# Optimization experiments

Hardware: AMD Instinct MI355X
Metric: run time of the kernel (lower is better)

The kernel has to match this reference:

```python
import jax, jax.numpy as jnp
import numpy as np

B, T, C, E = 16, 392, 512, 512
E8 = E // 8          # dim_project output
K = T // 2           # top_k / number of sampled positions
RECEPTIVE_FIELD = 2.0


def setup_inputs() -> dict:
    key = jax.random.key(0)
    ks = jax.random.split(key, 6)
    s = 0.03  # trunc_normal std used by the module init
    return {
        "x_in": jax.random.normal(ks[0], (B, T, C), jnp.float32),
        "W_dim": jax.random.normal(ks[1], (E8, E), jnp.float32) * s,
        "b_dim": jnp.zeros((E8,), jnp.float32),
        "W_time": jax.random.normal(ks[2], (T, T * T), jnp.float32) * s,
        "b_time": jnp.zeros((T,), jnp.float32),
        "W_offa": jax.random.normal(ks[3], (K, T), jnp.float32) * s,
        "W_offd": jax.random.normal(ks[4], (K, T), jnp.float32) * s,
    }


def _grid_sample_1d(x, idx_norm):
    """Bilinear 1D sample along last axis of x (b,T,c) at normalized coords
    idx_norm (b,K); padding_mode='border', align_corners=False.
    Equivalent to the module's F.grid_sample on (b,T,c,1) with grid (0, g)."""
    c = x.shape[-1]
    ix = ((idx_norm + 1.0) * c - 1.0) * 0.5          # unnormalize (align_corners=False)
    x0 = jnp.floor(ix)
    w1 = ix - x0                                     # fractional weight
    x0i = jnp.clip(x0.astype(jnp.int32), 0, c - 1)   # border clamp
    x1i = jnp.clip(x0.astype(jnp.int32) + 1, 0, c - 1)
    v0 = jnp.take_along_axis(x, x0i[:, None, :], axis=2)  # (b,T,K)
    v1 = jnp.take_along_axis(x, x1i[:, None, :], axis=2)
    return v0 * (1.0 - w1)[:, None, :] + v1 * w1[:, None, :]


def reference(x_in, W_dim, b_dim, W_time, b_time, W_offa, W_offd):
    b, t, c = x_in.shape
    scaler = 1.0 / E
    # dot-similarity attention map
    xi = jnp.einsum('btc,ec->bte', x_in, W_dim) + b_dim          # (b,t,E8)
    att = jax.nn.softmax(scaler * jnp.einsum('bie,bje->bij', xi, xi), axis=-1)
    # giant time projection: (b, t*t) @ (t*t, t)
    xt = att.reshape(b, t * t) @ W_time.T + b_time               # (b,t)
    off_a = jnp.tanh(xt @ W_offa.T) * RECEPTIVE_FIELD            # (b,K)
    off_d = jnp.tanh(xt @ W_offd.T) * RECEPTIVE_FIELD
    idx_a = jnp.arange(0, t, 2, dtype=jnp.float32)[None, :] + off_a
    idx_d = jnp.arange(1, t + 1, 2, dtype=jnp.float32)[None, :] + off_d
    # normalize_grid: n = K*2 = t
    denom = float(max(t - 1, 1))
    g_a = 2.0 * idx_a / denom - 1.0
    g_d = 2.0 * idx_d / denom - 1.0
    x_a = _grid_sample_1d(x_in, g_a)                             # (b,t,K)
    x_d = _grid_sample_1d(x_in, g_d)
    return (x_a, x_d)
```

## Files before the change

### kernel.cpp

```cpp
#include <hip/hip_runtime.h>
#include <hip/hip_bf16.h>

constexpr int BB   = 16;
constexpr int TT_  = 392;
constexpr int CC   = 512;
constexpr int E8_  = 64;
constexpr int KK   = 196;
constexpr long TT2 = 153664;
constexpr long OUT_HALF = 1229312;

constexpr int NC2   = 98;
constexpr int CH2   = 1568;
constexpr int BK2   = 224;
constexpr int NSTEP = 7;
constexpr int NJT   = 13;
constexpr int LDW = 228;
constexpr int LDX = 36;
constexpr int LDA = 68;

typedef __bf16 bf16_t;
typedef bf16_t bf16x8 __attribute__((ext_vector_type(8)));
typedef float  f32x4  __attribute__((ext_vector_type(4)));

static __device__ __forceinline__ unsigned int pk2(float a, float b) {
    unsigned short lo = __builtin_bit_cast(unsigned short, (bf16_t)a);
    unsigned short hi = __builtin_bit_cast(unsigned short, (bf16_t)b);
    return ((unsigned int)hi << 16) | (unsigned int)lo;
}
static __device__ __forceinline__ bf16x8 ld_frag(const bf16_t* p) {
    uint2 lo = *(const uint2*)p;
    uint2 hi = *(const uint2*)(p + 4);
    uint4 u = make_uint4(lo.x, lo.y, hi.x, hi.y);
    return __builtin_bit_cast(bf16x8, u);
}

__global__ __launch_bounds__(256) void k_xi(const float* __restrict__ x,
                                            const float* __restrict__ Wd,
                                            const float* __restrict__ bd,
                                            float* __restrict__ xi,
                                            float* __restrict__ xt) {
    __shared__ bf16_t Xl[64 * LDX];
    __shared__ bf16_t Wl[64 * LDX];
    int tid = threadIdx.x;
    if (blockIdx.x < 25) {
        int o = blockIdx.x * 256 + tid;
        if (o < BB * TT_) xt[o] = 0.f;
    }
    int m0 = blockIdx.x * 64;
    int wv = tid >> 6, lane = tid & 63;
    int n = lane & 15, quad = lane >> 4;
    f32x4 acc[4] = {};
    for (int kt = 0; kt < 16; ++kt) {
        __syncthreads();
        #pragma unroll
        for (int t = 0; t < 2; ++t) {
            int s = t * 256 + tid;
            int r = s >> 3, c4 = s & 7;
            f32x4 xv = *(const f32x4*)(x + (size_t)(m0 + r) * CC + kt * 32 + c4 * 4);
            f32x4 wq = *(const f32x4*)(Wd + (size_t)r * CC + kt * 32 + c4 * 4);
            *(uint2*)(&Xl[r * LDX + c4 * 4]) = make_uint2(pk2(xv.x, xv.y), pk2(xv.z, xv.w));
            *(uint2*)(&Wl[r * LDX + c4 * 4]) = make_uint2(pk2(wq.x, wq.y), pk2(wq.z, wq.w));
        }
        __syncthreads();
        bf16x8 a = ld_frag(&Xl[(wv * 16 + n) * LDX + quad * 8]);
        #pragma unroll
        for (int nt = 0; nt < 4; ++nt) {
            bf16x8 b = ld_frag(&Wl[(nt * 16 + n) * LDX + quad * 8]);
            acc[nt] = __builtin_amdgcn_mfma_f32_16x16x32_bf16(a, b, acc[nt], 0, 0, 0);
        }
    }
    #pragma unroll
    for (int nt = 0; nt < 4; ++nt)
        #pragma unroll
        for (int r = 0; r < 4; ++r) {
            int m = m0 + wv * 16 + quad * 4 + r;
            int e = nt * 16 + n;
            xi[(size_t)m * E8_ + e] = acc[nt][r] + bd[e];
        }
}

__global__ __launch_bounds__(256) void k_att(const float* __restrict__ xi,
                                             unsigned short* __restrict__ att_b) {
    __shared__ bf16_t Xb[400 * LDA];
    int b = blockIdx.x, tb = blockIdx.y;
    int tid = threadIdx.x;
    int wv = tid >> 6, lane = tid & 63;
    int n = lane & 15, quad = lane >> 4;
    #pragma unroll
    for (int t = 0; t < 25; ++t) {
        int s = t * 256 + tid;
        int r = s >> 4, c4 = s & 15;
        uint2 v = make_uint2(0u, 0u);
        if (r < TT_) {
            f32x4 xv = *(const f32x4*)(xi + (size_t)(b * TT_ + r) * E8_ + c4 * 4);
            v = make_uint2(pk2(xv.x, xv.y), pk2(xv.z, xv.w));
        }
        *(uint2*)(&Xb[r * LDA + c4 * 4]) = v;
    }
    __syncthreads();
    int arow = tb * 64 + wv * 16 + n;
    if (arow > 399) arow = 399;
    bf16x8 a0 = ld_frag(&Xb[arow * LDA + quad * 8]);
    bf16x8 a1 = ld_frag(&Xb[arow * LDA + 32 + quad * 8]);
    f32x4 acc[25];
    #pragma unroll
    for (int nt = 0; nt < 25; ++nt) acc[nt] = (f32x4){0.f, 0.f, 0.f, 0.f};
    #pragma unroll
    for (int nt = 0; nt < 25; ++nt) {
        bf16x8 b0 = ld_frag(&Xb[(nt * 16 + n) * LDA + quad * 8]);
        bf16x8 b1 = ld_frag(&Xb[(nt * 16 + n) * LDA + 32 + quad * 8]);
        acc[nt] = __builtin_amdgcn_mfma_f32_16x16x32_bf16(a0, b0, acc[nt], 0, 0, 0);
        acc[nt] = __builtin_amdgcn_mfma_f32_16x16x32_bf16(a1, b1, acc[nt], 0, 0, 0);
    }
    const float scaler = 1.0f / 512.0f;
    float mx[4] = {-1e30f, -1e30f, -1e30f, -1e30f};
    #pragma unroll
    for (int nt = 0; nt < 25; ++nt) {
        bool valid = (nt * 16 + n) < TT_;
        #pragma unroll
        for (int r = 0; r < 4; ++r) {
            float v = valid ? acc[nt][r] * scaler : -1e30f;
            acc[nt][r] = v;
            mx[r] = fmaxf(mx[r], v);
        }
    }
    #pragma unroll
    for (int r = 0; r < 4; ++r) {
        #pragma unroll
        for (int o = 1; o < 16; o <<= 1) mx[r] = fmaxf(mx[r], __shfl_xor(mx[r], o, 64));
    }
    float sm[4] = {0.f, 0.f, 0.f, 0.f};
    #pragma unroll
    for (int nt = 0; nt < 25; ++nt)
        #pragma unroll
        for (int r = 0; r < 4; ++r) {
            float e = __expf(acc[nt][r] - mx[r]);
            acc[nt][r] = e;
            sm[r] += e;
        }
    #pragma unroll
    for (int r = 0; r < 4; ++r) {
        #pragma unroll
        for (int o = 1; o < 16; o <<= 1) sm[r] += __shfl_xor(sm[r], o, 64);
        sm[r] = 1.0f / sm[r];
    }
    unsigned short* dst = att_b + (size_t)b * TT2;
    #pragma unroll
    for (int r = 0; r < 4; ++r) {
        int ti = tb * 64 + wv * 16 + quad * 4 + r;
        if (ti < TT_) {
            #pragma unroll
            for (int nt = 0; nt < 25; ++nt) {
                int tj = nt * 16 + n;
                if (tj < TT_)
                    dst[(size_t)ti * TT_ + tj] =
                        __builtin_bit_cast(unsigned short, (bf16_t)(acc[nt][r] * sm[r]));
            }
        }
    }
}

__global__ __launch_bounds__(128) void k_xt(const float* __restrict__ Wt,
                                            const unsigned short* __restrict__ att_b,
                                            float* __restrict__ xt) {
    __shared__ bf16_t Wl[32 * LDW];
    __shared__ bf16_t Al[16 * LDW];
    int c = blockIdx.x, jt = blockIdx.y;
    int tid = threadIdx.x;
    int wv = tid >> 6, lane = tid & 63;
    int n = lane & 15, quad = lane >> 4;
    f32x4 acc = {0.f, 0.f, 0.f, 0.f};
    long kbase = (long)c * CH2;
    for (int s = 0; s < NSTEP; ++s) {
        long k0 = kbase + (long)s * BK2;
        __syncthreads();
        #pragma unroll
        for (int t = 0; t < 14; ++t) {
            int idx = t * 128 + tid;
            int r = idx / 56, col = idx - r * 56;
            int jg = jt * 32 + r; if (jg > 391) jg = 391;
            f32x4 w = *(const f32x4*)(Wt + (size_t)jg * TT2 + k0 + col * 4);
            *(uint2*)(&Wl[r * LDW + col * 4]) = make_uint2(pk2(w.x, w.y), pk2(w.z, w.w));
        }
        #pragma unroll
        for (int t = 0; t < 4; ++t) {
            int idx = t * 128 + tid;
            if (idx < 448) {
                int r = idx / 28, q = idx - r * 28;
                uint4 v = *(const uint4*)(att_b + (size_t)r * TT2 + k0 + q * 8);
                *(uint2*)(&Al[r * LDW + q * 8])     = make_uint2(v.x, v.y);
                *(uint2*)(&Al[r * LDW + q * 8 + 4]) = make_uint2(v.z, v.w);
            }
        }
        __syncthreads();
        #pragma unroll
        for (int m = 0; m < 7; ++m) {
            int k = m * 32;
            bf16x8 a = ld_frag(&Al[n * LDW + k + quad * 8]);
            bf16x8 b = ld_frag(&Wl[(wv * 16 + n) * LDW + k + quad * 8]);
            acc = __builtin_amdgcn_mfma_f32_16x16x32_bf16(a, b, acc, 0, 0, 0);
        }
    }
    int j = jt * 32 + wv * 16 + n;
    if (j < TT_) {
        #pragma unroll
        for (int r = 0; r < 4; ++r) {
            int m = quad * 4 + r;
            unsafeAtomicAdd(&xt[(size_t)m * TT_ + j], acc[r]);
        }
    }
}

__global__ __launch_bounds__(256) void k_off(const float* __restrict__ xt,
                                             const float* __restrict__ bt,
                                             const float* __restrict__ Wa,
                                             const float* __restrict__ Wd,
                                             float* __restrict__ wix) {
    int o = blockIdx.x * 256 + threadIdx.x;
    if (o >= 2 * BB * KK) return;
    int which = o / (BB * KK);
    int rem = o - which * (BB * KK);
    int b = rem / KK;
    int k = rem - b * KK;
    const f32x4* __restrict__ wr = (const f32x4*)((which ? Wd : Wa) + (size_t)k * TT_);
    const f32x4* __restrict__ xr = (const f32x4*)(xt + (size_t)b * TT_);
    const f32x4* __restrict__ br = (const f32x4*)bt;
    float acc = 0.f;
    #pragma unroll 2
    for (int q = 0; q < TT_ / 4; ++q) {
        f32x4 w = wr[q], x = xr[q], bb = br[q];
        acc += (x.x + bb.x) * w.x + (x.y + bb.y) * w.y
             + (x.z + bb.z) * w.z + (x.w + bb.w) * w.w;
    }
    float off = tanhf(acc) * 2.0f;
    float idx = (float)(2 * k + which) + off;
    float g = 2.0f * idx / 391.0f - 1.0f;
    float ix = ((g + 1.0f) * 512.0f - 1.0f) * 0.5f;
    wix[o] = ix;
}

__global__ __launch_bounds__(256) void k_sample(const float* __restrict__ x,
                                                const float* __restrict__ wix,
                                                float* __restrict__ out) {
    __shared__ float xr[4][512];
    int b = blockIdx.x, t0 = blockIdx.y * 4;
    int tid = threadIdx.x;
    const float* src = x + ((size_t)b * TT_ + t0) * CC;
    #pragma unroll
    for (int s = 0; s < 2; ++s) {
        int idx = s * 256 + tid;
        ((f32x4*)xr)[idx] = ((const f32x4*)src)[idx];
    }
    __syncthreads();
    for (int w = tid; w < 2 * 4 * KK; w += 256) {
        int which = (w >= 4 * KK) ? 1 : 0;
        int rem = w - which * 4 * KK;
        int tl = rem / KK;
        int k = rem - tl * KK;
        float ix = wix[(size_t)which * (BB * KK) + b * KK + k];
        float x0f = floorf(ix);
        float w1 = ix - x0f;
        int c0 = (int)x0f;
        int c1 = c0 + 1;
        c0 = min(max(c0, 0), CC - 1);
        c1 = min(max(c1, 0), CC - 1);
        float v0 = xr[tl][c0], v1 = xr[tl][c1];
        out[(size_t)which * OUT_HALF + ((size_t)(b * TT_) + t0 + tl) * KK + k] =
            v0 * (1.0f - w1) + v1 * w1;
    }
}

extern "C" void kernel_launch(void* const* d_in, const int* in_sizes, int n_in,
                              void* d_out, int out_size, void* d_ws, size_t ws_size,
                              hipStream_t stream) {
    const float* x_in   = (const float*)d_in[0];
    const float* W_dim  = (const float*)d_in[1];
    const float* b_dim  = (const float*)d_in[2];
    const float* W_time = (const float*)d_in[3];
    const float* b_time = (const float*)d_in[4];
    const float* W_offa = (const float*)d_in[5];
    const float* W_offd = (const float*)d_in[6];
    float* out = (float*)d_out;
    float* ws  = (float*)d_ws;

    unsigned short* att_b = (unsigned short*)ws;
    float*          xi    = ws + 1229312;
    float*          xt    = ws + 1630720;
    float*          wix   = ws + 1636992;

    k_xi<<<98, 256, 0, stream>>>(x_in, W_dim, b_dim, xi, xt);
    k_att<<<dim3(BB, 7), 256, 0, stream>>>(xi, att_b);
    k_xt<<<dim3(NC2, NJT), 128, 0, stream>>>(W_time, att_b, xt);
    k_off<<<25, 256, 0, stream>>>(xt, b_time, W_offa, W_offd, wix);
    k_sample<<<dim3(BB, TT_ / 4), 256, 0, stream>>>(x_in, wix, out);
}
```

Before: 408.3 us.

## Double-buffer LDS staging in xi and xt GEMMs; store xi as bf16

Adds register-prefetch plus double-buffered shared memory to k_xi and k_xt, so the global loads for the next K step are issued before the MFMAs on the current buffer. This cuts the barrier count per step from two to one. It also makes k_xi write xi directly as bf16, which halves the traffic k_att reads. The cost is more registers (k_xt keeps 14 float4 plus 4 uint4 in flight, along with precomputed pointers) and twice the LDS, which may reduce occupancy.

```diff
diff --git a/kernel.cpp b/kernel.cpp
--- a/kernel.cpp
+++ b/kernel.cpp
@@ -37,10 +37,10 @@
 __global__ __launch_bounds__(256) void k_xi(const float* __restrict__ x,
                                             const float* __restrict__ Wd,
                                             const float* __restrict__ bd,
-                                            float* __restrict__ xi,
+                                            unsigned short* __restrict__ xi_b,
                                             float* __restrict__ xt) {
-    __shared__ bf16_t Xl[64 * LDX];
-    __shared__ bf16_t Wl[64 * LDX];
+    __shared__ bf16_t Xl[2][64 * LDX];
+    __shared__ bf16_t Wl[2][64 * LDX];
     int tid = threadIdx.x;
     if (blockIdx.x < 25) {
         int o = blockIdx.x * 256 + tid;
@@ -49,25 +49,44 @@
     int m0 = blockIdx.x * 64;
     int wv = tid >> 6, lane = tid & 63;
     int n = lane & 15, quad = lane >> 4;
+
+    int rr = tid >> 3, c4 = tid & 7;
+    const float* xsrc = x  + (size_t)(m0 + rr) * CC + c4 * 4;
+    const float* wsrc = Wd + (size_t)rr * CC + c4 * 4;
+    int dst = rr * LDX + c4 * 4;
+
+    f32x4 xv[2], wq[2];
+    auto LOADS = [&](int kt) {
+        #pragma unroll
+        for (int t = 0; t < 2; ++t) {
+            xv[t] = *(const f32x4*)(xsrc + (size_t)t * 32 * CC + kt * 32);
+            wq[t] = *(const f32x4*)(wsrc + (size_t)t * 32 * CC + kt * 32);
+        }
+    };
+    auto WRITE = [&](int p) {
+        #pragma unroll
+        for (int t = 0; t < 2; ++t) {
+            *(uint2*)(&Xl[p][dst + t * 32 * LDX]) =
+                make_uint2(pk2(xv[t].x, xv[t].y), pk2(xv[t].z, xv[t].w));
+            *(uint2*)(&Wl[p][dst + t * 32 * LDX]) =
+                make_uint2(pk2(wq[t].x, wq[t].y), pk2(wq[t].z, wq[t].w));
+        }
+    };
+
     f32x4 acc[4] = {};
+    LOADS(0); WRITE(0); __syncthreads();
+    int p = 0;
     for (int kt = 0; kt < 16; ++kt) {
+        if (kt + 1 < 16) LOADS(kt + 1);
+        bf16x8 a = ld_frag(&Xl[p][(wv * 16 + n) * LDX + quad * 8]);
+        #pragma unroll
+        for (int nt = 0; nt < 4; ++nt) {
+            bf16x8 b = ld_frag(&Wl[p][(nt * 16 + n) * LDX + quad * 8]);
+            acc[nt] = __builtin_amdgcn_mfma_f32_16x16x32_bf16(a, b, acc[nt], 0, 0, 0);
+        }
+        if (kt + 1 < 16) WRITE(p ^ 1);
         __syncthreads();
-        #pragma unroll
-        for (int t = 0; t < 2; ++t) {
-            int s = t * 256 + tid;
-            int r = s >> 3, c4 = s & 7;
-            f32x4 xv = *(const f32x4*)(x + (size_t)(m0 + r) * CC + kt * 32 + c4 * 4);
-            f32x4 wq = *(const f32x4*)(Wd + (size_t)r * CC + kt * 32 + c4 * 4);
-            *(uint2*)(&Xl[r * LDX + c4 * 4]) = make_uint2(pk2(xv.x, xv.y), pk2(xv.z, xv.w));
-            *(uint2*)(&Wl[r * LDX + c4 * 4]) = make_uint2(pk2(wq.x, wq.y), pk2(wq.z, wq.w));
-        }
-        __syncthreads();
-        bf16x8 a = ld_frag(&Xl[(wv * 16 + n) * LDX + quad * 8]);
-        #pragma unroll
-        for (int nt = 0; nt < 4; ++nt) {
-            bf16x8 b = ld_frag(&Wl[(nt * 16 + n) * LDX + quad * 8]);
-            acc[nt] = __builtin_amdgcn_mfma_f32_16x16x32_bf16(a, b, acc[nt], 0, 0, 0);
-        }
+        p ^= 1;
     }
     #pragma unroll
     for (int nt = 0; nt < 4; ++nt)
@@ -75,11 +94,12 @@
         for (int r = 0; r < 4; ++r) {
             int m = m0 + wv * 16 + quad * 4 + r;
             int e = nt * 16 + n;
-            xi[(size_t)m * E8_ + e] = acc[nt][r] + bd[e];
-        }
-}
-
-__global__ __launch_bounds__(256) void k_att(const float* __restrict__ xi,
+            xi_b[(size_t)m * E8_ + e] =
+                __builtin_bit_cast(unsigned short, (bf16_t)(acc[nt][r] + bd[e]));
+        }
+}
+
+__global__ __launch_bounds__(256) void k_att(const unsigned short* __restrict__ xi_b,
                                              unsigned short* __restrict__ att_b) {
     __shared__ bf16_t Xb[400 * LDA];
     int b = blockIdx.x, tb = blockIdx.y;
@@ -87,15 +107,19 @@
     int wv = tid >> 6, lane = tid & 63;
     int n = lane & 15, quad = lane >> 4;
     #pragma unroll
-    for (int t = 0; t < 25; ++t) {
+    for (int t = 0; t < 13; ++t) {
         int s = t * 256 + tid;
-        int r = s >> 4, c4 = s & 15;
-        uint2 v = make_uint2(0u, 0u);
-        if (r < TT_) {
-            f32x4 xv = *(const f32x4*)(xi + (size_t)(b * TT_ + r) * E8_ + c4 * 4);
-            v = make_uint2(pk2(xv.x, xv.y), pk2(xv.z, xv.w));
-        }
-        *(uint2*)(&Xb[r * LDA + c4 * 4]) = v;
+        if (s < 3200) {
+            int r = s >> 3, c8 = s & 7;
+            uint2 lo = make_uint2(0u, 0u), hi = make_uint2(0u, 0u);
+            if (r < TT_) {
+                uint4 v = *(const uint4*)(xi_b + ((size_t)(b * TT_ + r)) * E8_ + c8 * 8);
+                lo = make_uint2(v.x, v.y);
+                hi = make_uint2(v.z, v.w);
+            }
+            *(uint2*)(&Xb[r * LDA + c8 * 8])     = lo;
+            *(uint2*)(&Xb[r * LDA + c8 * 8 + 4]) = hi;
+        }
     }
     __syncthreads();
     int arow = tb * 64 + wv * 16 + n;
@@ -163,51 +187,79 @@
 __global__ __launch_bounds__(128) void k_xt(const float* __restrict__ Wt,
                                             const unsigned short* __restrict__ att_b,
                                             float* __restrict__ xt) {
-    __shared__ bf16_t Wl[32 * LDW];
-    __shared__ bf16_t Al[16 * LDW];
+    __shared__ bf16_t Wl[2][32 * LDW];
+    __shared__ bf16_t Al[2][16 * LDW];
     int c = blockIdx.x, jt = blockIdx.y;
     int tid = threadIdx.x;
     int wv = tid >> 6, lane = tid & 63;
     int n = lane & 15, quad = lane >> 4;
+    long kbase = (long)c * CH2;
+
+    const float* wsrc[14];
+    int wdst[14];
+    #pragma unroll
+    for (int t = 0; t < 14; ++t) {
+        int idx = t * 128 + tid;
+        int r = idx / 56, col = idx - r * 56;
+        int jg = jt * 32 + r; if (jg > 391) jg = 391;
+        wsrc[t] = Wt + (size_t)jg * TT2 + kbase + col * 4;
+        wdst[t] = r * LDW + col * 4;
+    }
+    const unsigned short* asrc[4];
+    int adst[4];
+    bool aok[4];
+    #pragma unroll
+    for (int t = 0; t < 4; ++t) {
+        int idx = t * 128 + tid;
+        aok[t] = idx < 448;
+        int r = aok[t] ? idx / 28 : 0;
+        int q = aok[t] ? idx - r * 28 : 0;
+        asrc[t] = att_b + (size_t)r * TT2 + kbase + q * 8;
+        adst[t] = r * LDW + q * 8;
+    }
+
+    f32x4 wb[14];
+    uint4 ab[4];
+    auto LOADS = [&](int s) {
+        long k0 = (long)s * BK2;
+        #pragma unroll
+        for (int t = 0; t < 14; ++t) wb[t] = *(const f32x4*)(wsrc[t] + k0);
+        #pragma unroll
+        for (int t = 0; t < 4; ++t) if (aok[t]) ab[t] = *(const uint4*)(asrc[t] + k0);
+    };
+    auto WRITE = [&](int p) {
+        #pragma unroll
+        for (int t = 0; t < 14; ++t)
+            *(uint2*)(&Wl[p][wdst[t]]) =
+                make_uint2(pk2(wb[t].x, wb[t].y), pk2(wb[t].z, wb[t].w));
+        #pragma unroll
+        for (int t = 0; t < 4; ++t) if (aok[t]) {
+            *(uint2*)(&Al[p][adst[t]])     = make_uint2(ab[t].x, ab[t].y);
+            *(uint2*)(&Al[p][adst[t] + 4]) = make_uint2(ab[t].z, ab[t].w);
+        }
+    };
+
     f32x4 acc = {0.f, 0.f, 0.f, 0.f};
-    long kbase = (long)c * CH2;
+    LOADS(0); WRITE(0); __syncthreads();
+    int p = 0;
     for (int s = 0; s < NSTEP; ++s) {
-        long k0 = kbase + (long)s * BK2;
-        __syncthreads();
-        #pragma unroll
-        for (int t = 0; t < 14; ++t) {
-            int idx = t * 128 + tid;
-            int r = idx / 56, col = idx - r * 56;
-            int jg = jt * 32 + r; if (jg > 391) jg = 391;
-            f32x4 w = *(const f32x4*)(Wt + (size_t)jg * TT2 + k0 + col * 4);
-            *(uint2*)(&Wl[r * LDW + col * 4]) = make_uint2(pk2(w.x, w.y), pk2(w.z, w.w));
-        }
-        #pragma unroll
-        for (int t = 0; t < 4; ++t) {
-            int idx = t * 128 + tid;
-            if (idx < 448) {
-                int r = idx / 28, q = idx - r * 28;
-                uint4 v = *(const uint4*)(att_b + (size_t)r * TT2 + k0 + q * 8);
-                *(uint2*)(&Al[r * LDW + q * 8])     = make_uint2(v.x, v.y);
-                *(uint2*)(&Al[r * LDW + q * 8 + 4]) = make_uint2(v.z, v.w);
-            }
-        }
-        __syncthreads();
+        if (s + 1 < NSTEP) LOADS(s + 1);
         #pragma unroll
         for (int m = 0; m < 7; ++m) {
             int k = m * 32;
-            bf16x8 a = ld_frag(&Al[n * LDW + k + quad * 8]);
-            bf16x8 b = ld_frag(&Wl[(wv * 16 + n) * LDW + k + quad * 8]);
+            bf16x8 a = ld_frag(&Al[p][n * LDW + k + quad * 8]);
+            bf16x8 b = ld_frag(&Wl[p][(wv * 16 + n) * LDW + k + quad * 8]);
             acc = __builtin_amdgcn_mfma_f32_16x16x32_bf16(a, b, acc, 0, 0, 0);
         }
+        if (s + 1 < NSTEP) WRITE(p ^ 1);
+        __syncthreads();
+        p ^= 1;
     }
     int j = jt * 32 + wv * 16 + n;
     if (j < TT_) {
         #pragma unroll
-        for (int r = 0; r < 4; ++r) {
-            int m = quad * 4 + r;
-            unsafeAtomicAdd(&xt[(size_t)m * TT_ + j], acc[r]);
-        }
+        for (int r = 0; r < 4; ++r)
+            unsafeAtomicAdd(&xt[(size_t)(quad * 4 + r) * TT_ + j], acc[r]);
     }
 }
 
@@ -284,12 +336,12 @@
     float* ws  = (float*)d_ws;
 
     unsigned short* att_b = (unsigned short*)ws;
-    float*          xi    = ws + 1229312;
+    unsigned short* xi_b  = (unsigned short*)(ws + 1229312);
     float*          xt    = ws + 1630720;
     float*          wix   = ws + 1636992;
 
-    k_xi<<<98, 256, 0, stream>>>(x_in, W_dim, b_dim, xi, xt);
-    k_att<<<dim3(BB, 7), 256, 0, stream>>>(xi, att_b);
+    k_xi<<<98, 256, 0, stream>>>(x_in, W_dim, b_dim, xi_b, xt);
+    k_att<<<dim3(BB, 7), 256, 0, stream>>>(xi_b, att_b);
     k_xt<<<dim3(NC2, NJT), 128, 0, stream>>>(W_time, att_b, xt);
     k_off<<<25, 256, 0, stream>>>(xt, b_time, W_offa, W_offd, wix);
     k_sample<<<dim3(BB, TT_ / 4), 256, 0, stream>>>(x_in, wix, out);
```

After: 404.8 us. No clear change (-0.9%).

## Load MFMA fragments directly from global with register prefetch, drop LDS staging

Applied to the files above, without the earlier changes.

The dominant k_xt kernel stops staging W_time and attention tiles through shared memory. Each wave now loads its MFMA fragments straight from global memory into registers, prefetching one step ahead, and blocks are remapped so consecutive K-chunks spread across XCDs. k_xi gets the same register-prefetch treatment and now writes xi as bf16, which halves the bytes k_att has to load. This removes LDS round-trips and __syncthreads barriers from a kernel bound by streaming W_time. The trade-off is that each lane reads only 32 bytes per row per step, so coalescing and cache behaviour depend on the hardware, and the atomics per output stay the same.

```diff
diff --git a/kernel.cpp b/kernel.cpp
--- a/kernel.cpp
+++ b/kernel.cpp
@@ -9,13 +9,10 @@
 constexpr long TT2 = 153664;
 constexpr long OUT_HALF = 1229312;
 
-constexpr int NC2   = 98;
-constexpr int CH2   = 1568;
-constexpr int BK2   = 224;
-constexpr int NSTEP = 7;
-constexpr int NJT   = 13;
-constexpr int LDW = 228;
-constexpr int LDX = 36;
+constexpr int NC2 = 98;
+constexpr int CH2 = 1568;
+constexpr int NJT16 = 25;
+
 constexpr int LDA = 68;
 
 typedef __bf16 bf16_t;
@@ -26,6 +23,10 @@
     unsigned short lo = __builtin_bit_cast(unsigned short, (bf16_t)a);
     unsigned short hi = __builtin_bit_cast(unsigned short, (bf16_t)b);
     return ((unsigned int)hi << 16) | (unsigned int)lo;
+}
+static __device__ __forceinline__ bf16x8 cvt8(f32x4 a, f32x4 b) {
+    uint4 u = make_uint4(pk2(a.x, a.y), pk2(a.z, a.w), pk2(b.x, b.y), pk2(b.z, b.w));
+    return __builtin_bit_cast(bf16x8, u);
 }
 static __device__ __forceinline__ bf16x8 ld_frag(const bf16_t* p) {
     uint2 lo = *(const uint2*)p;
@@ -37,49 +38,63 @@
 __global__ __launch_bounds__(256) void k_xi(const float* __restrict__ x,
                                             const float* __restrict__ Wd,
                                             const float* __restrict__ bd,
-                                            float* __restrict__ xi,
+                                            unsigned short* __restrict__ xi_b,
                                             float* __restrict__ xt) {
-    __shared__ bf16_t Xl[64 * LDX];
-    __shared__ bf16_t Wl[64 * LDX];
     int tid = threadIdx.x;
     if (blockIdx.x < 25) {
         int o = blockIdx.x * 256 + tid;
         if (o < BB * TT_) xt[o] = 0.f;
     }
-    int m0 = blockIdx.x * 64;
     int wv = tid >> 6, lane = tid & 63;
     int n = lane & 15, quad = lane >> 4;
+    int m = blockIdx.x * 64 + wv * 16 + n;
+    const float* xp = x  + (size_t)m * CC + quad * 8;
+    const float* wp = Wd + (size_t)n * CC + quad * 8;
+
     f32x4 acc[4] = {};
+    f32x4 a0c, a1c, b0c[4], b1c[4];
+    a0c = *(const f32x4*)xp;
+    a1c = *(const f32x4*)(xp + 4);
+    #pragma unroll
+    for (int nt = 0; nt < 4; ++nt) {
+        b0c[nt] = *(const f32x4*)(wp + (size_t)nt * 16 * CC);
+        b1c[nt] = *(const f32x4*)(wp + (size_t)nt * 16 * CC + 4);
+    }
     for (int kt = 0; kt < 16; ++kt) {
-        __syncthreads();
-        #pragma unroll
-        for (int t = 0; t < 2; ++t) {
-            int s = t * 256 + tid;
-            int r = s >> 3, c4 = s & 7;
-            f32x4 xv = *(const f32x4*)(x + (size_t)(m0 + r) * CC + kt * 32 + c4 * 4);
-            f32x4 wq = *(const f32x4*)(Wd + (size_t)r * CC + kt * 32 + c4 * 4);
-            *(uint2*)(&Xl[r * LDX + c4 * 4]) = make_uint2(pk2(xv.x, xv.y), pk2(xv.z, xv.w));
-            *(uint2*)(&Wl[r * LDX + c4 * 4]) = make_uint2(pk2(wq.x, wq.y), pk2(wq.z, wq.w));
-        }
-        __syncthreads();
-        bf16x8 a = ld_frag(&Xl[(wv * 16 + n) * LDX + quad * 8]);
+        f32x4 a0n, a1n, b0n[4], b1n[4];
+        if (kt < 15) {
+            a0n = *(const f32x4*)(xp + (kt + 1) * 32);
+            a1n = *(const f32x4*)(xp + (kt + 1) * 32 + 4);
+            #pragma unroll
+            for (int nt = 0; nt < 4; ++nt) {
+                b0n[nt] = *(const f32x4*)(wp + (size_t)nt * 16 * CC + (kt + 1) * 32);
+                b1n[nt] = *(const f32x4*)(wp + (size_t)nt * 16 * CC + (kt + 1) * 32 + 4);
+            }
+        }
+        bf16x8 a = cvt8(a0c, a1c);
         #pragma unroll
         for (int nt = 0; nt < 4; ++nt) {
-            bf16x8 b = ld_frag(&Wl[(nt * 16 + n) * LDX + quad * 8]);
+            bf16x8 b = cvt8(b0c[nt], b1c[nt]);
             acc[nt] = __builtin_amdgcn_mfma_f32_16x16x32_bf16(a, b, acc[nt], 0, 0, 0);
         }
+        if (kt < 15) {
+            a0c = a0n; a1c = a1n;
+            #pragma unroll
+            for (int nt = 0; nt < 4; ++nt) { b0c[nt] = b0n[nt]; b1c[nt] = b1n[nt]; }
+        }
     }
     #pragma unroll
     for (int nt = 0; nt < 4; ++nt)
         #pragma unroll
         for (int r = 0; r < 4; ++r) {
-            int m = m0 + wv * 16 + quad * 4 + r;
+            int mm = blockIdx.x * 64 + wv * 16 + quad * 4 + r;
             int e = nt * 16 + n;
-            xi[(size_t)m * E8_ + e] = acc[nt][r] + bd[e];
-        }
-}
-
-__global__ __launch_bounds__(256) void k_att(const float* __restrict__ xi,
+            xi_b[(size_t)mm * E8_ + e] =
+                __builtin_bit_cast(unsigned short, (bf16_t)(acc[nt][r] + bd[e]));
+        }
+}
+
+__global__ __launch_bounds__(256) void k_att(const unsigned short* __restrict__ xi_b,
                                              unsigned short* __restrict__ att_b) {
     __shared__ bf16_t Xb[400 * LDA];
     int b = blockIdx.x, tb = blockIdx.y;
@@ -87,15 +102,19 @@
     int wv = tid >> 6, lane = tid & 63;
     int n = lane & 15, quad = lane >> 4;
     #pragma unroll
-    for (int t = 0; t < 25; ++t) {
+    for (int t = 0; t < 13; ++t) {
         int s = t * 256 + tid;
-        int r = s >> 4, c4 = s & 15;
-        uint2 v = make_uint2(0u, 0u);
-        if (r < TT_) {
-            f32x4 xv = *(const f32x4*)(xi + (size_t)(b * TT_ + r) * E8_ + c4 * 4);
-            v = make_uint2(pk2(xv.x, xv.y), pk2(xv.z, xv.w));
-        }
-        *(uint2*)(&Xb[r * LDA + c4 * 4]) = v;
+        if (s < 3200) {
+            int r = s >> 3, c8 = s & 7;
+            uint2 lo = make_uint2(0u, 0u), hi = make_uint2(0u, 0u);
+            if (r < TT_) {
+                uint4 v = *(const uint4*)(xi_b + ((size_t)(b * TT_ + r)) * E8_ + c8 * 8);
+                lo = make_uint2(v.x, v.y);
+                hi = make_uint2(v.z, v.w);
+            }
+            *(uint2*)(&Xb[r * LDA + c8 * 8])     = lo;
+            *(uint2*)(&Xb[r * LDA + c8 * 8 + 4]) = hi;
+        }
     }
     __syncthreads();
     int arow = tb * 64 + wv * 16 + n;
@@ -160,54 +179,47 @@
     }
 }
 
-__global__ __launch_bounds__(128) void k_xt(const float* __restrict__ Wt,
+__global__ __launch_bounds__(256) void k_xt(const float* __restrict__ Wt,
                                             const unsigned short* __restrict__ att_b,
                                             float* __restrict__ xt) {
-    __shared__ bf16_t Wl[32 * LDW];
-    __shared__ bf16_t Al[16 * LDW];
-    int c = blockIdx.x, jt = blockIdx.y;
+    int wg = blockIdx.x;
+    int xcd = wg & 7, s = wg >> 3;
+    int cidx = s / 7, jt4 = s - cidx * 7;
+    int c = cidx * 8 + xcd;
+    if (c >= NC2) return;
     int tid = threadIdx.x;
     int wv = tid >> 6, lane = tid & 63;
     int n = lane & 15, quad = lane >> 4;
+    int jt = jt4 * 4 + wv;
+    if (jt >= NJT16) return;
+    int j = jt * 16 + n;
+    int jl = j < TT_ ? j : TT_ - 1;
+    long kbase = (long)c * CH2;
+    const unsigned short* ap = att_b + (size_t)n * TT2 + kbase + quad * 8;
+    const float*          wp = Wt + (size_t)jl * TT2 + kbase + quad * 8;
+
     f32x4 acc = {0.f, 0.f, 0.f, 0.f};
-    long kbase = (long)c * CH2;
-    for (int s = 0; s < NSTEP; ++s) {
-        long k0 = kbase + (long)s * BK2;
-        __syncthreads();
-        #pragma unroll
-        for (int t = 0; t < 14; ++t) {
-            int idx = t * 128 + tid;
-            int r = idx / 56, col = idx - r * 56;
-            int jg = jt * 32 + r; if (jg > 391) jg = 391;
-            f32x4 w = *(const f32x4*)(Wt + (size_t)jg * TT2 + k0 + col * 4);
-            *(uint2*)(&Wl[r * LDW + col * 4]) = make_uint2(pk2(w.x, w.y), pk2(w.z, w.w));
-        }
-        #pragma unroll
-        for (int t = 0; t < 4; ++t) {
-            int idx = t * 128 + tid;
-            if (idx < 448) {
-                int r = idx / 28, q = idx - r * 28;
-                uint4 v = *(const uint4*)(att_b + (size_t)r * TT2 + k0 + q * 8);
-                *(uint2*)(&Al[r * LDW + q * 8])     = make_uint2(v.x, v.y);
-                *(uint2*)(&Al[r * LDW + q * 8 + 4]) = make_uint2(v.z, v.w);
-            }
-        }
-        __syncthreads();
-        #pragma unroll
-        for (int m = 0; m < 7; ++m) {
-            int k = m * 32;
-            bf16x8 a = ld_frag(&Al[n * LDW + k + quad * 8]);
-            bf16x8 b = ld_frag(&Wl[(wv * 16 + n) * LDW + k + quad * 8]);
-            acc = __builtin_amdgcn_mfma_f32_16x16x32_bf16(a, b, acc, 0, 0, 0);
-        }
-    }
-    int j = jt * 32 + wv * 16 + n;
+    uint4 ac; f32x4 w0c, w1c;
+    ac  = *(const uint4*)ap;
+    w0c = *(const f32x4*)wp;
+    w1c = *(const f32x4*)(wp + 4);
+    for (int m = 0; m < 49; ++m) {
+        uint4 an; f32x4 w0n, w1n;
+        if (m < 48) {
+            ac.w = ac.w;
+            an  = *(const uint4*)(ap + (m + 1) * 32);
+            w0n = *(const f32x4*)(wp + (m + 1) * 32);
+            w1n = *(const f32x4*)(wp + (m + 1) * 32 + 4);
+        }
+        bf16x8 a = __builtin_bit_cast(bf16x8, ac);
+        bf16x8 b = cvt8(w0c, w1c);
+        acc = __builtin_amdgcn_mfma_f32_16x16x32_bf16(a, b, acc, 0, 0, 0);
+        if (m < 48) { ac = an; w0c = w0n; w1c = w1n; }
+    }
     if (j < TT_) {
         #pragma unroll
-        for (int r = 0; r < 4; ++r) {
-            int m = quad * 4 + r;
-            unsafeAtomicAdd(&xt[(size_t)m * TT_ + j], acc[r]);
-        }
+        for (int r = 0; r < 4; ++r)
+            unsafeAtomicAdd(&xt[(size_t)(quad * 4 + r) * TT_ + j], acc[r]);
     }
 }
 
@@ -284,13 +296,13 @@
     float* ws  = (float*)d_ws;
 
     unsigned short* att_b = (unsigned short*)ws;
-    float*          xi    = ws + 1229312;
+    unsigned short* xi_b  = (unsigned short*)(ws + 1229312);
     float*          xt    = ws + 1630720;
     float*          wix   = ws + 1636992;
 
-    k_xi<<<98, 256, 0, stream>>>(x_in, W_dim, b_dim, xi, xt);
-    k_att<<<dim3(BB, 7), 256, 0, stream>>>(xi, att_b);
-    k_xt<<<dim3(NC2, NJT), 128, 0, stream>>>(W_time, att_b, xt);
+    k_xi<<<98, 256, 0, stream>>>(x_in, W_dim, b_dim, xi_b, xt);
+    k_att<<<dim3(BB, 7), 256, 0, stream>>>(xi_b, att_b);
+    k_xt<<<728, 256, 0, stream>>>(W_time, att_b, xt);
     k_off<<<25, 256, 0, stream>>>(xt, b_time, W_offa, W_offd, wix);
     k_sample<<<dim3(BB, TT_ / 4), 256, 0, stream>>>(x_in, wix, out);
 }
```

After: 411.8 us. Within noise of the previous version (+0.9%).
